# Performance work log

Measured on AMD Instinct MI355X. Metric: run time of the kernel, lower is better.

The kernel has to match this reference:

```python
import jax, jax.numpy as jnp
import numpy as np
from jax import lax

BS, L, NB = 16, 50, 64          # batch, seq_length, num_blk_pervisit
D = 256                          # d_model
BLK_D = 768                      # frozen block-embedding dim
N_BLK = 65536                    # block vocab size
MEM_SIZE = 64                    # mem_size == mem_update_size (required for stackable memory)
MEM_UPDATE = 64
EPS = 1e-5


def _blk_trans(x, w1, b1, w2, b2, g, b):
    # Linear(768->2D) + ReLU + Linear(2D->D) + LayerNorm(D); dropout omitted (eval mode)
    h = jax.nn.relu(x @ w1 + b1)
    y = h @ w2 + b2
    mu = jnp.mean(y, axis=-1, keepdims=True)
    var = jnp.mean((y - mu) ** 2, axis=-1, keepdims=True)
    return g * (y - mu) * lax.rsqrt(var + EPS) + b


def setup_inputs() -> dict:
    key = jax.random.key(0)
    ks = jax.random.split(key, 16)
    s = 0.02
    f32 = jnp.float32
    return {
        "v_all": jax.random.normal(ks[0], (BS, L, D), f32),
        "transformed_v_all": jax.random.normal(ks[1], (BS, L, D), f32),
        "blk_emb_w": jax.random.normal(ks[2], (N_BLK, BLK_D), f32) * s,
        "bt_w1": jax.random.normal(ks[3], (BLK_D, 2 * D), f32) * s,
        "bt_b1": jnp.zeros((2 * D,), f32),
        "bt_w2": jax.random.normal(ks[4], (2 * D, D), f32) * s,
        "bt_b2": jnp.zeros((D,), f32),
        "bt_g": jnp.ones((D,), f32),
        "bt_b": jnp.zeros((D,), f32),
        "wq": jax.random.normal(ks[5], (D, D), f32) * s,
        "wk": jax.random.normal(ks[6], (D, D), f32) * s,
        "am_w1": jax.random.normal(ks[7], (2 * D, D), f32) * s,
        "am_b1": jnp.zeros((D,), f32),
        "am_w2": jax.random.normal(ks[8], (D, 1), f32) * s,
        "out_w": jax.random.normal(ks[9], (2 * D, 2), f32) * s,
        "out_b": jnp.zeros((2,), f32),
        "input_txt": jax.random.randint(ks[10], (BS, L, NB), 0, N_BLK, dtype=jnp.int32),
        "masks_txt": jax.random.randint(ks[11], (BS, L, NB), 0, 2, dtype=jnp.int32),
        "lengths": jax.random.randint(ks[12], (BS,), 2, L + 1, dtype=jnp.int32),
    }


def reference(v_all, transformed_v_all, blk_emb_w, bt_w1, bt_b1, bt_w2, bt_b2,
              bt_g, bt_b, wq, wk, am_w1, am_b1, am_w2, out_w, out_b,
              input_txt, masks_txt, lengths):
    bt = (bt_w1, bt_b1, bt_w2, bt_b2, bt_g, bt_b)

    # --- per-visit block selection (att_mlp + topk gather) ---
    v_text = _blk_trans(blk_emb_w[input_txt], *bt)                 # [BS,L,NB,D]
    tv = jnp.broadcast_to(transformed_v_all[:, :, None, :], v_text.shape)
    att_in = jnp.concatenate([tv, v_text], axis=-1)                # [BS,L,NB,2D]
    score = (jnp.tanh(att_in @ am_w1 + am_b1) @ am_w2)[..., 0]     # [BS,L,NB]
    score = jax.nn.softmax(score, axis=-1)
    score = jnp.where(masks_txt == 0, 0.0, score)
    idx = lax.top_k(score, MEM_UPDATE)[1]                          # [BS,L,MU]
    sel_ids = jnp.take_along_axis(input_txt, idx, axis=2)          # [BS,L,MU]
    sel_mask = jnp.take_along_axis(masks_txt, idx, axis=2)

    # --- sequential memory update recurrence ---
    query = transformed_v_all + v_all                              # [BS,L,D]
    scale = jnp.sqrt(jnp.float32(D))

    def step(carry, xs):
        ids, mk = carry                                            # [BS, M]
        nids, nmk, q = xs                                          # [BS,MU], [BS,MU], [BS,D]
        mem_in = jnp.concatenate([ids, nids], axis=1)              # [BS, 2M]
        mask_in = jnp.concatenate([mk, nmk], axis=1)
        x = _blk_trans(blk_emb_w[mem_in], *bt)                     # [BS,2M,D]
        e = jnp.einsum("bd,bmd->bm", q @ wq, x @ wk) / scale
        att = jnp.where(mask_in == 0, 0.0, jax.nn.softmax(e, axis=-1))
        tki = lax.top_k(att, MEM_SIZE)[1]                          # [BS, M]
        oi = jnp.take_along_axis(mem_in, tki, axis=1)
        om = jnp.take_along_axis(mask_in, tki, axis=1)
        return (oi, om), oi

    xs = (jnp.swapaxes(sel_ids[:, 1:], 0, 1),
          jnp.swapaxes(sel_mask[:, 1:], 0, 1),
          jnp.swapaxes(query[:, 1:], 0, 1))
    _, ys = lax.scan(step, (sel_ids[:, 0], sel_mask[:, 0]), xs)    # [L-1,BS,M]
    mem_stack = jnp.swapaxes(ys, 0, 1)                             # [BS,L-1,M] == memory[1:]
    memory_final = jnp.take_along_axis(
        mem_stack, (lengths - 2)[:, None, None], axis=1)[:, 0]      # [BS,M]

    # --- pooling + output head ---
    vmask = jnp.arange(L)[None, :] < lengths[:, None]              # length-masked max pool
    v_final = jnp.max(jnp.where(vmask[:, :, None], transformed_v_all, -jnp.inf), axis=1)
    mem_vec_final = jnp.max(_blk_trans(blk_emb_w[memory_final], *bt), axis=1)
    output = jnp.concatenate([v_final, mem_vec_final], axis=1) @ out_w + out_b
    return (output, memory_final)
```

## Files before the change

kernel.cpp:

```cpp
#include <hip/hip_runtime.h>
#include <math.h>

constexpr int kBS   = 16;
constexpr int kL    = 50;
constexpr int kNB   = 64;
constexpr int kD    = 256;
constexpr int kNBLK = 65536;
constexpr int kMaxUsed = 51200;
constexpr int kChunk   = 25600;

#define NEG_HUGE (-3.402823466e38f)

typedef _Float16 h8 __attribute__((ext_vector_type(8)));
typedef float f32x4 __attribute__((ext_vector_type(4)));

__device__ __forceinline__ unsigned f2sort(float f) {
    unsigned u = __float_as_uint(f);
    return (u & 0x80000000u) ? ~u : (u | 0x80000000u);
}

__device__ __forceinline__ void bitonic_u64(unsigned long long* s, int i, int n) {
    for (int k = 2; k <= n; k <<= 1) {
        for (int j = k >> 1; j > 0; j >>= 1) {
            __syncthreads();
            int ixj = i ^ j;
            if (ixj > i) {
                unsigned long long x = s[i], y = s[ixj];
                bool sw = ((i & k) == 0) ? (x > y) : (x < y);
                if (sw) { s[i] = y; s[ixj] = x; }
            }
        }
    }
    __syncthreads();
}

__global__ void k_clear(int* __restrict__ flags) {
    flags[blockIdx.x * 256 + threadIdx.x] = 0;
}
__global__ void k_mark(const int* __restrict__ ids, int* __restrict__ flags, int n) {
    int i = blockIdx.x * 256 + threadIdx.x;
    if (i < n) flags[ids[i]] = 1;
}
__global__ void k_scan_a(const int* __restrict__ flags, int* __restrict__ slots,
                         int* __restrict__ bsum) {
    int i = blockIdx.x * 256 + threadIdx.x;
    __shared__ int s[256];
    int v = flags[i];
    s[threadIdx.x] = v; __syncthreads();
    for (int o = 1; o < 256; o <<= 1) {
        int t2 = (threadIdx.x >= o) ? s[threadIdx.x - o] : 0;
        __syncthreads();
        s[threadIdx.x] += t2;
        __syncthreads();
    }
    slots[i] = s[threadIdx.x] - v;
    if (threadIdx.x == 255) bsum[blockIdx.x] = s[255];
}
__global__ void k_scan_b(int* __restrict__ bsum, int* __restrict__ mcount) {
    __shared__ int s[256];
    int v = bsum[threadIdx.x];
    s[threadIdx.x] = v; __syncthreads();
    for (int o = 1; o < 256; o <<= 1) {
        int t2 = (threadIdx.x >= o) ? s[threadIdx.x - o] : 0;
        __syncthreads();
        s[threadIdx.x] += t2;
        __syncthreads();
    }
    bsum[threadIdx.x] = s[threadIdx.x] - v;
    if (threadIdx.x == 255) *mcount = s[255];
}
__global__ void k_scan_c(const int* __restrict__ flags, int* __restrict__ slots,
                         const int* __restrict__ bsum, int* __restrict__ ulist) {
    int i = blockIdx.x * 256 + threadIdx.x;
    int slot = slots[i] + bsum[blockIdx.x];
    slots[i] = slot;
    if (flags[i]) ulist[slot] = i;
}

__global__ void k_split_bT(const float* __restrict__ B, int ldb, int K,
                           _Float16* __restrict__ Ph, _Float16* __restrict__ Pl,
                           int row_off, int ldp, float scale)
{
    int n = blockIdx.x;
    for (int k = threadIdx.x; k < K; k += 256) {
        float v = B[(long long)k * ldb + n] * scale;
        _Float16 h = (_Float16)v;
        _Float16 l = (_Float16)(v - (float)h);
        Ph[(long long)(row_off + n) * ldp + k] = h;
        Pl[(long long)(row_off + n) * ldp + k] = l;
    }
}

__global__ void k_split_gatherA(const float* __restrict__ emb, const int* __restrict__ ulist,
                                const int* __restrict__ mcount, int chunk_off,
                                _Float16* __restrict__ Ph, _Float16* __restrict__ Pl,
                                float scale)
{
    int r = blockIdx.x;
    if (chunk_off + r >= *mcount) return;
    long long id = ulist[chunk_off + r];
    const float* src = emb + id * 768;
    #pragma unroll
    for (int j = 0; j < 3; ++j) {
        int c = threadIdx.x + j * 256;
        float v = src[c] * scale;
        _Float16 h = (_Float16)v;
        Ph[(long long)r * 768 + c] = h;
        Pl[(long long)r * 768 + c] = (_Float16)(v - (float)h);
    }
}

__global__ void k_split_plainA(const float* __restrict__ A, const float* __restrict__ A2,
                               _Float16* __restrict__ Ph, _Float16* __restrict__ Pl,
                               float scale)
{
    int r = blockIdx.x, c = threadIdx.x;
    float v = A[(long long)r * 256 + c];
    if (A2) v += A2[(long long)r * 256 + c];
    v *= scale;
    _Float16 h = (_Float16)v;
    Ph[(long long)r * 256 + c] = h;
    Pl[(long long)r * 256 + c] = (_Float16)(v - (float)h);
}

template<int NFR>
__global__ __launch_bounds__(512) void gemm_f16p(
    const _Float16* __restrict__ Ah, const _Float16* __restrict__ Al,
    const _Float16* __restrict__ Bh, const _Float16* __restrict__ Bl,
    float* __restrict__ C, int ldc,
    _Float16* __restrict__ Ch, _Float16* __restrict__ Cl,
    int Mstatic, const int* __restrict__ mcount, int moff,
    int K, const float* __restrict__ bias, int relu,
    float inv_scale, float out_scale)
{
    constexpr int N  = NFR * 64;
    constexpr int NS = NFR / 2;
    int mlim = Mstatic;
    if (mcount) mlim = *mcount - moff;
    const int bm = blockIdx.x * 128;
    if (bm >= mlim) return;

    __shared__ _Float16 Ash[128][40];
    __shared__ _Float16 Asl[128][40];
    __shared__ _Float16 Bsh[N][40];
    __shared__ _Float16 Bsl[N][40];

    const int t = threadIdx.x;
    const int lane = t & 63, wid = t >> 6;
    const int wm = wid >> 2, wn = wid & 3;
    const int fr = lane & 15, fk = (lane >> 4) * 8;

    const int rowA = t >> 2;
    const int kOff = (t & 3) * 8;
    const _Float16* aph = Ah + (long long)(bm + rowA) * K + kOff;
    const _Float16* apl = Al + (long long)(bm + rowA) * K + kOff;
    const _Float16* bph[NS];
    const _Float16* bpl[NS];
    #pragma unroll
    for (int s = 0; s < NS; ++s) {
        int r = rowA + s * 128;
        bph[s] = Bh + (long long)r * K + kOff;
        bpl[s] = Bl + (long long)r * K + kOff;
    }

    f32x4 acc[4][NFR];
    #pragma unroll
    for (int m = 0; m < 4; ++m)
        #pragma unroll
        for (int n = 0; n < NFR; ++n)
            acc[m][n] = (f32x4){0.f, 0.f, 0.f, 0.f};

    h8 pah = *(const h8*)aph;
    h8 pal = *(const h8*)apl;
    h8 pbh[NS], pbl[NS];
    #pragma unroll
    for (int s = 0; s < NS; ++s) { pbh[s] = *(const h8*)bph[s]; pbl[s] = *(const h8*)bpl[s]; }

    const int nt = K / 32;
    for (int tI = 0; tI < nt; ++tI) {
        __syncthreads();
        *(h8*)&Ash[rowA][kOff] = pah;
        *(h8*)&Asl[rowA][kOff] = pal;
        #pragma unroll
        for (int s = 0; s < NS; ++s) {
            *(h8*)&Bsh[rowA + s * 128][kOff] = pbh[s];
            *(h8*)&Bsl[rowA + s * 128][kOff] = pbl[s];
        }
        __syncthreads();
        if (tI + 1 < nt) {
            int k0 = (tI + 1) * 32;
            pah = *(const h8*)(aph + k0);
            pal = *(const h8*)(apl + k0);
            #pragma unroll
            for (int s = 0; s < NS; ++s) {
                pbh[s] = *(const h8*)(bph[s] + k0);
                pbl[s] = *(const h8*)(bpl[s] + k0);
            }
        }
        h8 ah_[4], al_[4];
        #pragma unroll
        for (int m = 0; m < 4; ++m) {
            ah_[m] = *(const h8*)&Ash[wm * 64 + m * 16 + fr][fk];
            al_[m] = *(const h8*)&Asl[wm * 64 + m * 16 + fr][fk];
        }
        #pragma unroll
        for (int n = 0; n < NFR; ++n) {
            h8 bh_ = *(const h8*)&Bsh[wn * (NFR * 16) + n * 16 + fr][fk];
            h8 bl_ = *(const h8*)&Bsl[wn * (NFR * 16) + n * 16 + fr][fk];
            #pragma unroll
            for (int m = 0; m < 4; ++m) {
                acc[m][n] = __builtin_amdgcn_mfma_f32_16x16x32_f16(ah_[m], bh_, acc[m][n], 0, 0, 0);
                acc[m][n] = __builtin_amdgcn_mfma_f32_16x16x32_f16(ah_[m], bl_, acc[m][n], 0, 0, 0);
                acc[m][n] = __builtin_amdgcn_mfma_f32_16x16x32_f16(al_[m], bh_, acc[m][n], 0, 0, 0);
            }
        }
    }

    const int cr0 = (lane >> 4) * 4;
    #pragma unroll
    for (int m = 0; m < 4; ++m) {
        #pragma unroll
        for (int r = 0; r < 4; ++r) {
            int row = bm + wm * 64 + m * 16 + cr0 + r;
            if (row >= mlim) continue;
            #pragma unroll
            for (int n = 0; n < NFR; ++n) {
                int col = wn * (NFR * 16) + n * 16 + fr;
                float v = acc[m][n][r] * inv_scale;
                if (bias) v += bias[col];
                if (relu) v = fmaxf(v, 0.f);
                if (Ch) {
                    float w = v * out_scale;
                    _Float16 hh = (_Float16)w;
                    Ch[(long long)row * N + col] = hh;
                    Cl[(long long)row * N + col] = (_Float16)(w - (float)hh);
                } else {
                    C[(long long)row * ldc + col] = v;
                }
            }
        }
    }
}

__global__ __launch_bounds__(256) void ln256_split(
    float* __restrict__ Y, const float* __restrict__ g, const float* __restrict__ b,
    int Mstatic, const int* __restrict__ mcount,
    _Float16* __restrict__ Ph, _Float16* __restrict__ Pl, float pscale)
{
    int row = blockIdx.x;
    int mlim = mcount ? *mcount : Mstatic;
    if (row >= mlim) return;
    int d = threadIdx.x;
    float v = Y[(long long)row * 256 + d];
    __shared__ float red[256];
    red[d] = v; __syncthreads();
    for (int off = 128; off; off >>= 1) { if (d < off) red[d] += red[d + off]; __syncthreads(); }
    float mu = red[0] * (1.f / 256.f);
    __syncthreads();
    float dv = v - mu;
    red[d] = dv * dv; __syncthreads();
    for (int off = 128; off; off >>= 1) { if (d < off) red[d] += red[d + off]; __syncthreads(); }
    float var = red[0] * (1.f / 256.f);
    float out = g[d] * dv * (1.f / sqrtf(var + 1e-5f)) + b[d];
    Y[(long long)row * 256 + d] = out;
    float w = out * pscale;
    _Float16 hh = (_Float16)w;
    Ph[(long long)row * 256 + d] = hh;
    Pl[(long long)row * 256 + d] = (_Float16)(w - (float)hh);
}

__global__ __launch_bounds__(256) void p1score(
    const float* __restrict__ tvp, const float* __restrict__ AK,
    const int* __restrict__ slots, const float* __restrict__ am_w2,
    const int* __restrict__ ids, float* __restrict__ scores)
{
    int bl = blockIdx.x;
    int lane = threadIdx.x & 63;
    int wv   = threadIdx.x >> 6;
    float4 tv = *(const float4*)(tvp + (long long)bl * 256 + lane * 4);
    float4 w2 = *(const float4*)(am_w2 + lane * 4);
    for (int s = wv * 16; s < wv * 16 + 16; ++s) {
        int slot = slots[ids[bl * 64 + s]];
        float4 a = *(const float4*)(AK + (long long)slot * 512 + lane * 4);
        double p = (double)tanhf(tv.x + a.x) * w2.x
                 + (double)tanhf(tv.y + a.y) * w2.y
                 + (double)tanhf(tv.z + a.z) * w2.z
                 + (double)tanhf(tv.w + a.w) * w2.w;
        #pragma unroll
        for (int off = 32; off; off >>= 1) p += __shfl_down(p, off);
        if (lane == 0) scores[bl * 64 + s] = (float)p;
    }
}

__global__ __launch_bounds__(64) void p1sort(
    const float* __restrict__ scores, const int* __restrict__ ids_in,
    const int* __restrict__ mk_in, int* __restrict__ sel_ids, int* __restrict__ sel_mk)
{
    int bl = blockIdx.x;
    int i = threadIdx.x;
    __shared__ unsigned long long s[64];
    float sc = scores[bl * 64 + i];
    int mk = mk_in[bl * 64 + i];
    float key = mk ? sc : NEG_HUGE;
    s[i] = ((unsigned long long)(~f2sort(key)) << 32) | (unsigned)i;
    bitonic_u64(s, i, 64);
    int src = (int)(unsigned)(s[i] & 0xffffffffull);
    sel_ids[bl * 64 + i] = ids_in[bl * 64 + src];
    sel_mk [bl * 64 + i] = mk_in [bl * 64 + src];
}

__global__ __launch_bounds__(256) void etab2(
    const float* __restrict__ qw, const float* __restrict__ AK,
    const int* __restrict__ slots, const int* __restrict__ sel_ids,
    float* __restrict__ E)
{
    const int l = blockIdx.x;
    const int b = blockIdx.y;
    __shared__ float Ks[16][64];
    __shared__ float Qs[16][68];
    __shared__ int rowA[64];
    const int t  = threadIdx.x;
    const int tx = t & 15, ty = t >> 4;
    if (t < 64) rowA[t] = slots[sel_ids[(b * kL + l) * 64 + t]];
    __syncthreads();

    const int rA = t >> 2;
    const int kA = (t & 3) * 4;
    const float* aptr = AK + (long long)rowA[rA] * 512 + 256 + kA;
    const float* qbase = qw + ((long long)b * kL + 1) * 256;
    const bool tsok = rA < 49;

    double acc[4][4];
    #pragma unroll
    for (int i = 0; i < 4; ++i)
        #pragma unroll
        for (int j = 0; j < 4; ++j) acc[i][j] = 0.0;

    for (int k0 = 0; k0 < 256; k0 += 16) {
        float4 av = *(const float4*)(aptr + k0);
        float4 bv = make_float4(0.f, 0.f, 0.f, 0.f);
        if (tsok) bv = *(const float4*)(qbase + (long long)rA * 256 + k0 + kA);
        __syncthreads();
        Ks[kA + 0][rA] = av.x; Ks[kA + 1][rA] = av.y;
        Ks[kA + 2][rA] = av.z; Ks[kA + 3][rA] = av.w;
        Qs[kA + 0][rA] = bv.x; Qs[kA + 1][rA] = bv.y;
        Qs[kA + 2][rA] = bv.z; Qs[kA + 3][rA] = bv.w;
        __syncthreads();
        #pragma unroll
        for (int k = 0; k < 16; ++k) {
            float a[4], q[4];
            *(float4*)&a[0] = *(const float4*)&Ks[k][tx * 4];
            *(float4*)&q[0] = *(const float4*)&Qs[k][ty * 4];
            #pragma unroll
            for (int i = 0; i < 4; ++i)
                #pragma unroll
                for (int j = 0; j < 4; ++j)
                    acc[i][j] += (double)a[i] * (double)q[j];
        }
    }
    #pragma unroll
    for (int j = 0; j < 4; ++j) {
        int ts = ty * 4 + j;
        if (ts >= 49) continue;
        #pragma unroll
        for (int i = 0; i < 4; ++i) {
            int s = tx * 4 + i;
            E[((long long)b * 49 + ts) * 3200 + l * 64 + s] = (float)acc[i][j];
        }
    }
}

__global__ __launch_bounds__(64) void recur(
    const float* __restrict__ E, const int* __restrict__ sel_ids,
    const int* __restrict__ sel_mk, const int* __restrict__ lengths,
    int* __restrict__ memf, float* __restrict__ dout_mem)
{
    const int b = blockIdx.x;
    const int lane = threadIdx.x;

    int cid = sel_ids[(b * kL) * 64 + lane];
    int cmk = sel_mk [(b * kL) * 64 + lane];
    int ccd = lane;

    const int tlast = lengths[b] - 2;
    const float* Eb = E + (long long)b * 49 * 3200;

    for (int ts = 0; ts <= tlast; ++ts) {
        int nid = sel_ids[(b * kL + ts + 1) * 64 + lane];
        int nmk = sel_mk [(b * kL + ts + 1) * 64 + lane];
        const float* Et = Eb + (long long)ts * 3200;

        float k0 = cmk ? Et[ccd] : NEG_HUGE;
        float k1 = nmk ? Et[(ts + 1) * 64 + lane] : NEG_HUGE;
        unsigned long long s0 = ((unsigned long long)(~f2sort(k0)) << 32) | (unsigned)lane;
        unsigned long long s1 = ((unsigned long long)(~f2sort(k1)) << 32) | (unsigned)(64 + lane);

        #pragma unroll
        for (int k = 2; k <= 128; k <<= 1) {
            #pragma unroll
            for (int j = k >> 1; j > 0; j >>= 1) {
                if (j == 64) {
                    unsigned long long mn = s0 < s1 ? s0 : s1;
                    unsigned long long mx = s0 < s1 ? s1 : s0;
                    s0 = mn; s1 = mx;
                } else {
                    bool up   = (lane & j) == 0;
                    bool asc0 = (lane & k) == 0;
                    bool asc1 = (((lane + 64) & k) == 0);
                    unsigned long long p0 = __shfl_xor(s0, j, 64);
                    unsigned long long p1 = __shfl_xor(s1, j, 64);
                    bool km0 = (asc0 == up), km1 = (asc1 == up);
                    s0 = (km0 == (s0 < p0)) ? s0 : p0;
                    s1 = (km1 == (s1 < p1)) ? s1 : p1;
                }
            }
        }

        int src  = (int)(unsigned)(s0 & 0xffffffffull);
        int srcl = src & 63;
        int c_id = __shfl(cid, srcl, 64);
        int c_mk = __shfl(cmk, srcl, 64);
        int c_cd = __shfl(ccd, srcl, 64);
        int n_id = __shfl(nid, srcl, 64);
        int n_mk = __shfl(nmk, srcl, 64);
        bool isnew = src >= 64;
        cid = isnew ? n_id : c_id;
        cmk = isnew ? n_mk : c_mk;
        ccd = isnew ? ((ts + 1) * 64 + srcl) : c_cd;
    }

    memf[b * 64 + lane] = cid;
    dout_mem[b * 64 + lane] = (float)cid;
}

__global__ __launch_bounds__(256) void head_k(
    const float* __restrict__ tva, const int* __restrict__ lengths,
    const float* __restrict__ T, const int* __restrict__ slots,
    const int* __restrict__ memf, const float* __restrict__ out_w,
    const float* __restrict__ out_b, float* __restrict__ dout)
{
    int b = blockIdx.x, d = threadIdx.x;
    int len = lengths[b];
    float vf = NEG_HUGE;
    for (int l = 0; l < len; ++l) vf = fmaxf(vf, tva[((long long)b * kL + l) * 256 + d]);
    float mv = NEG_HUGE;
    for (int m = 0; m < 64; ++m) {
        int slot = slots[memf[b * 64 + m]];
        mv = fmaxf(mv, T[(long long)slot * 256 + d]);
    }
    double p0 = (double)vf * out_w[d * 2 + 0] + (double)mv * out_w[(256 + d) * 2 + 0];
    double p1 = (double)vf * out_w[d * 2 + 1] + (double)mv * out_w[(256 + d) * 2 + 1];
    __shared__ double r0[256], r1[256];
    r0[d] = p0; r1[d] = p1; __syncthreads();
    for (int off = 128; off; off >>= 1) {
        if (d < off) { r0[d] += r0[d + off]; r1[d] += r1[d + off]; }
        __syncthreads();
    }
    if (d == 0) {
        dout[b * 2 + 0] = (float)(r0[0] + out_b[0]);
        dout[b * 2 + 1] = (float)(r1[0] + out_b[1]);
    }
}

extern "C" void kernel_launch(void* const* d_in, const int* in_sizes, int n_in,
                              void* d_out, int out_size, void* d_ws, size_t ws_size,
                              hipStream_t stream)
{
    const float* v_all  = (const float*)d_in[0];
    const float* tva    = (const float*)d_in[1];
    const float* emb    = (const float*)d_in[2];
    const float* bt_w1  = (const float*)d_in[3];
    const float* bt_b1  = (const float*)d_in[4];
    const float* bt_w2  = (const float*)d_in[5];
    const float* bt_b2  = (const float*)d_in[6];
    const float* bt_g   = (const float*)d_in[7];
    const float* bt_bb  = (const float*)d_in[8];
    const float* wq     = (const float*)d_in[9];
    const float* wk     = (const float*)d_in[10];
    const float* am_w1  = (const float*)d_in[11];
    const float* am_b1  = (const float*)d_in[12];
    const float* am_w2  = (const float*)d_in[13];
    const float* out_w  = (const float*)d_in[14];
    const float* out_b  = (const float*)d_in[15];
    const int*   in_txt = (const int*)d_in[16];
    const int*   mk_txt = (const int*)d_in[17];
    const int*   lens   = (const int*)d_in[18];
    float* dout = (float*)d_out;

    const float S12 = 4096.f, S7 = 128.f, S8 = 256.f;
    const float INV24 = 1.f / 16777216.f;
    const float INV19 = 1.f / 524288.f;
    const float INV20 = 1.f / 1048576.f;

    size_t off = 0;
    float* W = (float*)d_ws;
    auto take = [&](size_t n) { float* p = W + off; off += (n + 3) & ~(size_t)3; return p; };
    auto takeh = [&](size_t nh) { return (_Float16*)take((nh + 1) / 2); };

    float* AKp  = take((size_t)kMaxUsed * 512);
    float* Tt   = take((size_t)kMaxUsed * 256);
    _Float16* Hph = takeh((size_t)kMaxUsed * 512);
    _Float16* Hpl = takeh((size_t)kMaxUsed * 512);
    _Float16* Tth = takeh((size_t)kMaxUsed * 256);
    _Float16* Ttl = takeh((size_t)kMaxUsed * 256);
    float* Ep   = take((size_t)16 * 49 * 3200);
    float* tvpP = take((size_t)800 * 256);
    float* qwP  = take((size_t)800 * 256);
    float* scP  = take((size_t)800 * 64);
    int*   selI = (int*)take((size_t)800 * 64);
    int*   selM = (int*)take((size_t)800 * 64);
    int*   flagsP = (int*)take(kNBLK);
    int*   slotsP = (int*)take(kNBLK);
    int*   ulist  = (int*)take(kNBLK);
    int*   bsum   = (int*)take(256);
    int*   mcount = (int*)take(16);
    int*   memfP  = (int*)take(1024);
    _Float16* W1h = takeh((size_t)512 * 768);
    _Float16* W1l = takeh((size_t)512 * 768);
    _Float16* W2h = takeh((size_t)256 * 512);
    _Float16* W2l = takeh((size_t)256 * 512);
    _Float16* BCh = takeh((size_t)512 * 256);
    _Float16* BCl = takeh((size_t)512 * 256);
    _Float16* ALh = takeh((size_t)256 * 256);
    _Float16* ALl = takeh((size_t)256 * 256);
    _Float16* WQh = takeh((size_t)256 * 256);
    _Float16* WQl = takeh((size_t)256 * 256);
    _Float16* TAh = takeh((size_t)896 * 256);
    _Float16* TAl = takeh((size_t)896 * 256);
    _Float16* QAh = takeh((size_t)896 * 256);
    _Float16* QAl = takeh((size_t)896 * 256);
    _Float16* Aeh = (_Float16*)AKp;
    _Float16* Ael = Aeh + (size_t)kChunk * 768;

    k_clear<<<dim3(256), dim3(256), 0, stream>>>(flagsP);
    k_mark <<<dim3(200), dim3(256), 0, stream>>>(in_txt, flagsP, 51200);
    k_scan_a<<<dim3(256), dim3(256), 0, stream>>>(flagsP, slotsP, bsum);
    k_scan_b<<<dim3(1),   dim3(256), 0, stream>>>(bsum, mcount);
    k_scan_c<<<dim3(256), dim3(256), 0, stream>>>(flagsP, slotsP, bsum, ulist);
    k_split_bT<<<dim3(512), dim3(256), 0, stream>>>(bt_w1, 512, 768, W1h, W1l, 0, 768, S12);
    k_split_bT<<<dim3(256), dim3(256), 0, stream>>>(bt_w2, 256, 512, W2h, W2l, 0, 512, S12);
    k_split_bT<<<dim3(256), dim3(256), 0, stream>>>(am_w1 + 256 * 256, 256, 256, BCh, BCl, 0,   256, S12);
    k_split_bT<<<dim3(256), dim3(256), 0, stream>>>(wk,                256, 256, BCh, BCl, 256, 256, S12);
    k_split_bT<<<dim3(256), dim3(256), 0, stream>>>(am_w1, 256, 256, ALh, ALl, 0, 256, S12);
    k_split_bT<<<dim3(256), dim3(256), 0, stream>>>(wq,    256, 256, WQh, WQl, 0, 256, S12);
    k_split_plainA<<<dim3(800), dim3(256), 0, stream>>>(tva, nullptr, TAh, TAl, S7);
    k_split_plainA<<<dim3(800), dim3(256), 0, stream>>>(tva, v_all,  QAh, QAl, S7);

    gemm_f16p<4><<<dim3(7), dim3(512), 0, stream>>>(
        TAh, TAl, ALh, ALl, tvpP, 256, nullptr, nullptr,
        800, nullptr, 0, 256, am_b1, 0, INV19, 1.f);
    gemm_f16p<4><<<dim3(7), dim3(512), 0, stream>>>(
        QAh, QAl, WQh, WQl, qwP, 256, nullptr, nullptr,
        800, nullptr, 0, 256, nullptr, 0, INV19, 1.f);

    for (int c = 0; c < 2; ++c) {
        k_split_gatherA<<<dim3(kChunk), dim3(256), 0, stream>>>(
            emb, ulist, mcount, c * kChunk, Aeh, Ael, S12);
        gemm_f16p<8><<<dim3(kChunk / 128), dim3(512), 0, stream>>>(
            Aeh, Ael, W1h, W1l, nullptr, 0,
            Hph + (size_t)c * kChunk * 512, Hpl + (size_t)c * kChunk * 512,
            0, mcount, c * kChunk, 768, bt_b1, 1, INV24, S12);
    }
    gemm_f16p<4><<<dim3(kMaxUsed / 128), dim3(512), 0, stream>>>(
        Hph, Hpl, W2h, W2l, Tt, 256, nullptr, nullptr,
        0, mcount, 0, 512, bt_b2, 0, INV24, 1.f);
    ln256_split<<<dim3(kMaxUsed), dim3(256), 0, stream>>>(
        Tt, bt_g, bt_bb, 0, mcount, Tth, Ttl, S8);
    gemm_f16p<8><<<dim3(kMaxUsed / 128), dim3(512), 0, stream>>>(
        Tth, Ttl, BCh, BCl, AKp, 512, nullptr, nullptr,
        0, mcount, 0, 256, nullptr, 0, INV20, 1.f);

    p1score<<<dim3(800), dim3(256), 0, stream>>>(tvpP, AKp, slotsP, am_w2, in_txt, scP);
    p1sort<<<dim3(800), dim3(64), 0, stream>>>(scP, in_txt, mk_txt, selI, selM);

    etab2<<<dim3(50, 16), dim3(256), 0, stream>>>(qwP, AKp, slotsP, selI, Ep);

    recur<<<dim3(16), dim3(64), 0, stream>>>(Ep, selI, selM, lens, memfP, dout + 32);

    head_k<<<dim3(16), dim3(256), 0, stream>>>(tva, lens, Tt, slotsP, memfP,
                                               out_w, out_b, dout);
}
```

Before: 704.3 us.

## Retile split-fp16 GEMM to 128x128 tiles with 2D grid over N

Replaces the templated GEMM, where each 512-thread block covered 128 rows by the full N width (256 or 512), with a fixed 128x128 tile kernel of 256 threads and a 2D grid over N. This gives more, smaller blocks for better occupancy and load balance across CUs, and lowers per-block LDS and register pressure. In exchange each A tile is reloaded from global memory once per N tile, which adds A traffic for the wide GEMMs.

```diff
diff --git a/kernel.cpp b/kernel.cpp
--- a/kernel.cpp
+++ b/kernel.cpp
@@ -123,90 +123,76 @@
     Pl[(long long)r * 256 + c] = (_Float16)(v - (float)h);
 }
 
-template<int NFR>
-__global__ __launch_bounds__(512) void gemm_f16p(
+__global__ __launch_bounds__(256) void gemm_p128(
     const _Float16* __restrict__ Ah, const _Float16* __restrict__ Al,
     const _Float16* __restrict__ Bh, const _Float16* __restrict__ Bl,
     float* __restrict__ C, int ldc,
-    _Float16* __restrict__ Ch, _Float16* __restrict__ Cl,
+    _Float16* __restrict__ Ch, _Float16* __restrict__ Cl, int ldch,
     int Mstatic, const int* __restrict__ mcount, int moff,
     int K, const float* __restrict__ bias, int relu,
     float inv_scale, float out_scale)
 {
-    constexpr int N  = NFR * 64;
-    constexpr int NS = NFR / 2;
     int mlim = Mstatic;
     if (mcount) mlim = *mcount - moff;
     const int bm = blockIdx.x * 128;
     if (bm >= mlim) return;
+    const int bn = blockIdx.y * 128;
 
     __shared__ _Float16 Ash[128][40];
     __shared__ _Float16 Asl[128][40];
-    __shared__ _Float16 Bsh[N][40];
-    __shared__ _Float16 Bsl[N][40];
+    __shared__ _Float16 Bsh[128][40];
+    __shared__ _Float16 Bsl[128][40];
 
     const int t = threadIdx.x;
     const int lane = t & 63, wid = t >> 6;
-    const int wm = wid >> 2, wn = wid & 3;
+    const int wr = (wid >> 1) * 64, wc = (wid & 1) * 64;
     const int fr = lane & 15, fk = (lane >> 4) * 8;
 
-    const int rowA = t >> 2;
-    const int kOff = (t & 3) * 8;
-    const _Float16* aph = Ah + (long long)(bm + rowA) * K + kOff;
-    const _Float16* apl = Al + (long long)(bm + rowA) * K + kOff;
-    const _Float16* bph[NS];
-    const _Float16* bpl[NS];
-    #pragma unroll
-    for (int s = 0; s < NS; ++s) {
-        int r = rowA + s * 128;
-        bph[s] = Bh + (long long)r * K + kOff;
-        bpl[s] = Bl + (long long)r * K + kOff;
-    }
-
-    f32x4 acc[4][NFR];
+    const int r0 = t >> 2;
+    const int ko = (t & 3) * 8;
+    const _Float16* aph = Ah + (long long)(bm + r0) * K + ko;
+    const _Float16* apl = Al + (long long)(bm + r0) * K + ko;
+    const _Float16* bph = Bh + (long long)(bn + r0) * K + ko;
+    const _Float16* bpl = Bl + (long long)(bn + r0) * K + ko;
+    const long long step64 = (long long)64 * K;
+
+    f32x4 acc[4][4];
     #pragma unroll
     for (int m = 0; m < 4; ++m)
         #pragma unroll
-        for (int n = 0; n < NFR; ++n)
+        for (int n = 0; n < 4; ++n)
             acc[m][n] = (f32x4){0.f, 0.f, 0.f, 0.f};
 
-    h8 pah = *(const h8*)aph;
-    h8 pal = *(const h8*)apl;
-    h8 pbh[NS], pbl[NS];
-    #pragma unroll
-    for (int s = 0; s < NS; ++s) { pbh[s] = *(const h8*)bph[s]; pbl[s] = *(const h8*)bpl[s]; }
+    h8 pah0 = *(const h8*)aph,  pah1 = *(const h8*)(aph + step64);
+    h8 pal0 = *(const h8*)apl,  pal1 = *(const h8*)(apl + step64);
+    h8 pbh0 = *(const h8*)bph,  pbh1 = *(const h8*)(bph + step64);
+    h8 pbl0 = *(const h8*)bpl,  pbl1 = *(const h8*)(bpl + step64);
 
     const int nt = K / 32;
     for (int tI = 0; tI < nt; ++tI) {
         __syncthreads();
-        *(h8*)&Ash[rowA][kOff] = pah;
-        *(h8*)&Asl[rowA][kOff] = pal;
-        #pragma unroll
-        for (int s = 0; s < NS; ++s) {
-            *(h8*)&Bsh[rowA + s * 128][kOff] = pbh[s];
-            *(h8*)&Bsl[rowA + s * 128][kOff] = pbl[s];
-        }
+        *(h8*)&Ash[r0][ko]      = pah0;  *(h8*)&Ash[r0 + 64][ko] = pah1;
+        *(h8*)&Asl[r0][ko]      = pal0;  *(h8*)&Asl[r0 + 64][ko] = pal1;
+        *(h8*)&Bsh[r0][ko]      = pbh0;  *(h8*)&Bsh[r0 + 64][ko] = pbh1;
+        *(h8*)&Bsl[r0][ko]      = pbl0;  *(h8*)&Bsl[r0 + 64][ko] = pbl1;
         __syncthreads();
         if (tI + 1 < nt) {
             int k0 = (tI + 1) * 32;
-            pah = *(const h8*)(aph + k0);
-            pal = *(const h8*)(apl + k0);
-            #pragma unroll
-            for (int s = 0; s < NS; ++s) {
-                pbh[s] = *(const h8*)(bph[s] + k0);
-                pbl[s] = *(const h8*)(bpl[s] + k0);
-            }
+            pah0 = *(const h8*)(aph + k0); pah1 = *(const h8*)(aph + step64 + k0);
+            pal0 = *(const h8*)(apl + k0); pal1 = *(const h8*)(apl + step64 + k0);
+            pbh0 = *(const h8*)(bph + k0); pbh1 = *(const h8*)(bph + step64 + k0);
+            pbl0 = *(const h8*)(bpl + k0); pbl1 = *(const h8*)(bpl + step64 + k0);
         }
         h8 ah_[4], al_[4];
         #pragma unroll
         for (int m = 0; m < 4; ++m) {
-            ah_[m] = *(const h8*)&Ash[wm * 64 + m * 16 + fr][fk];
-            al_[m] = *(const h8*)&Asl[wm * 64 + m * 16 + fr][fk];
-        }
-        #pragma unroll
-        for (int n = 0; n < NFR; ++n) {
-            h8 bh_ = *(const h8*)&Bsh[wn * (NFR * 16) + n * 16 + fr][fk];
-            h8 bl_ = *(const h8*)&Bsl[wn * (NFR * 16) + n * 16 + fr][fk];
+            ah_[m] = *(const h8*)&Ash[wr + m * 16 + fr][fk];
+            al_[m] = *(const h8*)&Asl[wr + m * 16 + fr][fk];
+        }
+        #pragma unroll
+        for (int n = 0; n < 4; ++n) {
+            h8 bh_ = *(const h8*)&Bsh[wc + n * 16 + fr][fk];
+            h8 bl_ = *(const h8*)&Bsl[wc + n * 16 + fr][fk];
             #pragma unroll
             for (int m = 0; m < 4; ++m) {
                 acc[m][n] = __builtin_amdgcn_mfma_f32_16x16x32_f16(ah_[m], bh_, acc[m][n], 0, 0, 0);
@@ -221,19 +207,19 @@
     for (int m = 0; m < 4; ++m) {
         #pragma unroll
         for (int r = 0; r < 4; ++r) {
-            int row = bm + wm * 64 + m * 16 + cr0 + r;
+            int row = bm + wr + m * 16 + cr0 + r;
             if (row >= mlim) continue;
             #pragma unroll
-            for (int n = 0; n < NFR; ++n) {
-                int col = wn * (NFR * 16) + n * 16 + fr;
+            for (int n = 0; n < 4; ++n) {
+                int col = bn + wc + n * 16 + fr;
                 float v = acc[m][n][r] * inv_scale;
                 if (bias) v += bias[col];
                 if (relu) v = fmaxf(v, 0.f);
                 if (Ch) {
                     float w = v * out_scale;
                     _Float16 hh = (_Float16)w;
-                    Ch[(long long)row * N + col] = hh;
-                    Cl[(long long)row * N + col] = (_Float16)(w - (float)hh);
+                    Ch[(long long)row * ldch + col] = hh;
+                    Cl[(long long)row * ldch + col] = (_Float16)(w - (float)hh);
                 } else {
                     C[(long long)row * ldc + col] = v;
                 }
@@ -546,28 +532,28 @@
     k_split_plainA<<<dim3(800), dim3(256), 0, stream>>>(tva, nullptr, TAh, TAl, S7);
     k_split_plainA<<<dim3(800), dim3(256), 0, stream>>>(tva, v_all,  QAh, QAl, S7);
 
-    gemm_f16p<4><<<dim3(7), dim3(512), 0, stream>>>(
-        TAh, TAl, ALh, ALl, tvpP, 256, nullptr, nullptr,
+    gemm_p128<<<dim3(7, 2), dim3(256), 0, stream>>>(
+        TAh, TAl, ALh, ALl, tvpP, 256, nullptr, nullptr, 0,
         800, nullptr, 0, 256, am_b1, 0, INV19, 1.f);
-    gemm_f16p<4><<<dim3(7), dim3(512), 0, stream>>>(
-        QAh, QAl, WQh, WQl, qwP, 256, nullptr, nullptr,
+    gemm_p128<<<dim3(7, 2), dim3(256), 0, stream>>>(
+        QAh, QAl, WQh, WQl, qwP, 256, nullptr, nullptr, 0,
         800, nullptr, 0, 256, nullptr, 0, INV19, 1.f);
 
     for (int c = 0; c < 2; ++c) {
         k_split_gatherA<<<dim3(kChunk), dim3(256), 0, stream>>>(
             emb, ulist, mcount, c * kChunk, Aeh, Ael, S12);
-        gemm_f16p<8><<<dim3(kChunk / 128), dim3(512), 0, stream>>>(
+        gemm_p128<<<dim3(kChunk / 128, 4), dim3(256), 0, stream>>>(
             Aeh, Ael, W1h, W1l, nullptr, 0,
-            Hph + (size_t)c * kChunk * 512, Hpl + (size_t)c * kChunk * 512,
+            Hph + (size_t)c * kChunk * 512, Hpl + (size_t)c * kChunk * 512, 512,
             0, mcount, c * kChunk, 768, bt_b1, 1, INV24, S12);
     }
-    gemm_f16p<4><<<dim3(kMaxUsed / 128), dim3(512), 0, stream>>>(
-        Hph, Hpl, W2h, W2l, Tt, 256, nullptr, nullptr,
+    gemm_p128<<<dim3(kMaxUsed / 128, 2), dim3(256), 0, stream>>>(
+        Hph, Hpl, W2h, W2l, Tt, 256, nullptr, nullptr, 0,
         0, mcount, 0, 512, bt_b2, 0, INV24, 1.f);
     ln256_split<<<dim3(kMaxUsed), dim3(256), 0, stream>>>(
         Tt, bt_g, bt_bb, 0, mcount, Tth, Ttl, S8);
-    gemm_f16p<8><<<dim3(kMaxUsed / 128), dim3(512), 0, stream>>>(
-        Tth, Ttl, BCh, BCl, AKp, 512, nullptr, nullptr,
+    gemm_p128<<<dim3(kMaxUsed / 128, 4), dim3(256), 0, stream>>>(
+        Tth, Ttl, BCh, BCl, AKp, 512, nullptr, nullptr, 0,
         0, mcount, 0, 256, nullptr, 0, INV20, 1.f);
 
     p1score<<<dim3(800), dim3(256), 0, stream>>>(tvpP, AKp, slotsP, am_w2, in_txt, scP);
```

Result: faster. 640.9 us (-9.0%).
